# Kernel tuning notes

Measured on AMD Instinct MI355X. Metric: run time of the kernel, lower is better.

Reference implementation:

```python
import jax, jax.numpy as jnp
import numpy as np

EPS = 1e-5
NUM_HEADS = 8
POOL_K = 50
POOL_S = 15
DEPTH = 4


def _conv2d(x, w, b, pad_h, pad_w):
    y = jax.lax.conv_general_dilated(
        x, w, window_strides=(1, 1),
        padding=((pad_h, pad_h), (pad_w, pad_w)),
        dimension_numbers=('NCHW', 'OIHW', 'NCHW'))
    return y + b[None, :, None, None]


def _bn_eval(x, g, b):
    # eval-mode BatchNorm2d with running_mean=0, running_var=1
    s = g / jnp.sqrt(1.0 + EPS)
    return x * s[None, :, None, None] + b[None, :, None, None]


def _layernorm(x, g, b):
    m = x.mean(-1, keepdims=True)
    v = ((x - m) ** 2).mean(-1, keepdims=True)
    return (x - m) / jnp.sqrt(v + EPS) * g + b


def _mha(x, wq, bq, wk, bk, wv, bv, wo, bo):
    B, n, d = x.shape
    def split(h):
        return h.reshape(B, n, NUM_HEADS, -1).transpose(0, 2, 1, 3)  # b h n dk
    q = split(x @ wq.T + bq)
    k = split(x @ wk.T + bk)
    v = split(x @ wv.T + bv)
    dk = q.shape[-1]
    scores = jnp.einsum('bhqd,bhkd->bhqk', q, k) / jnp.sqrt(jnp.float32(dk))
    attn = jax.nn.softmax(scores, axis=-1)
    o = jnp.einsum('bhqk,bhkd->bhqd', attn, v).transpose(0, 2, 1, 3).reshape(B, n, d)
    return o @ wo.T + bo


def _encoder(x, p):
    (g1, b1, g2, b2, wq, bq, wk, bk, wv, bv, wo, bo, f1w, f1b, f2w, f2b) = p
    h = _layernorm(x, g1, b1)
    x = x + _mha(h, wq, bq, wk, bk, wv, bv, wo, bo)
    h = _layernorm(x, g2, b2)
    ff = jax.nn.gelu(h @ f1w.T + f1b, approximate=False) @ f2w.T + f2b
    return x + ff


def _forward(x, tw1, tb1, tw2, tb2, tw3, tb3, tw4, tb4, bn1_g, bn1_b, sw, sb,
             bn2_g, bn2_b, ln1_g, ln1_b, ln2_g, ln2_b, wq, bq, wk, bk, wv, bv,
             wo, bo, f1w, f1b, f2w, f2b, ew, eb, bn3_g, bn3_b, cw, cb):
    B, C, T = x.shape
    xi = x[:, None]  # [B,1,C,T]
    h = jnp.concatenate([
        _conv2d(xi, tw1, tb1, 0, 7),
        _conv2d(xi, tw2, tb2, 0, 12),
        _conv2d(xi, tw3, tb3, 0, 25),
        _conv2d(xi, tw4, tb4, 0, 32)], axis=1)          # [B,D,C,T]
    h = _bn_eval(h, bn1_g, bn1_b)
    h = _conv2d(h, sw, sb, 0, 0)                         # [B,D,1,T]
    h = jax.nn.elu(_bn_eval(h, bn2_g, bn2_b))[:, :, 0]   # [B,D,T]

    npos = (T - POOL_K) // POOL_S + 1
    idx = np.arange(npos)[:, None] * POOL_S + np.arange(POOL_K)  # [n,K]
    win = h[:, :, idx]                                   # [B,D,n,K]
    avg = win.mean(-1)                                   # [B,D,n]
    var = win.var(-1, ddof=1)                            # unbiased, like torch
    vlog = jnp.log(jnp.clip(var, 1e-6, 1e6))
    x1 = avg.transpose(0, 2, 1)                          # [B,n,D]
    x2 = vlog.transpose(0, 2, 1)

    for i in range(DEPTH):
        p = (ln1_g[i], ln1_b[i], ln2_g[i], ln2_b[i], wq[i], bq[i], wk[i], bk[i],
             wv[i], bv[i], wo[i], bo[i], f1w[i], f1b[i], f2w[i], f2b[i])
        x1 = _encoder(x1, p)
        x2 = _encoder(x2, p)

    h = jnp.concatenate([x1[:, :, None, :], x2[:, :, None, :]], axis=2)  # [B,n,2,D]
    h = jax.nn.elu(_bn_eval(_conv2d(h, ew, eb, 0, 0), bn3_g, bn3_b))     # [B,n,1,D]
    return h.reshape(B, -1) @ cw.T + cb


def setup_inputs() -> dict:
    B, C, T, D, n, ff, ncls = 16, 64, 1000, 128, 64, 512, 4
    ks = iter(jax.random.split(jax.random.key(0), 48))
    def nrm(shape, s=0.02):
        return jax.random.normal(next(ks), shape, jnp.float32) * s
    inp = {
        'x': jax.random.normal(next(ks), (B, C, T), jnp.float32),
        'tw1': nrm((D // 4, 1, 1, 15)), 'tb1': jnp.zeros(D // 4),
        'tw2': nrm((D // 4, 1, 1, 25)), 'tb2': jnp.zeros(D // 4),
        'tw3': nrm((D // 4, 1, 1, 51)), 'tb3': jnp.zeros(D // 4),
        'tw4': nrm((D // 4, 1, 1, 65)), 'tb4': jnp.zeros(D // 4),
        'bn1_g': jnp.ones(D), 'bn1_b': jnp.zeros(D),
        'sw': nrm((D, D, C, 1)), 'sb': jnp.zeros(D),
        'bn2_g': jnp.ones(D), 'bn2_b': jnp.zeros(D),
        'ln1_g': jnp.ones((DEPTH, D)), 'ln1_b': jnp.zeros((DEPTH, D)),
        'ln2_g': jnp.ones((DEPTH, D)), 'ln2_b': jnp.zeros((DEPTH, D)),
        'wq': nrm((DEPTH, D, D)), 'bq': jnp.zeros((DEPTH, D)),
        'wk': nrm((DEPTH, D, D)), 'bk': jnp.zeros((DEPTH, D)),
        'wv': nrm((DEPTH, D, D)), 'bv': jnp.zeros((DEPTH, D)),
        'wo': nrm((DEPTH, D, D)), 'bo': jnp.zeros((DEPTH, D)),
        'f1w': nrm((DEPTH, ff, D)), 'f1b': jnp.zeros((DEPTH, ff)),
        'f2w': nrm((DEPTH, D, ff)), 'f2b': jnp.zeros((DEPTH, D)),
        'ew': nrm((n, n, 2, 1)), 'eb': jnp.zeros(n),
        'bn3_g': jnp.ones(n), 'bn3_b': jnp.zeros(n),
        'cw': nrm((ncls, D * n)), 'cb': jnp.zeros(ncls),
    }
    return inp


def reference(x, tw1, tb1, tw2, tb2, tw3, tb3, tw4, tb4, bn1_g, bn1_b, sw, sb,
              bn2_g, bn2_b, ln1_g, ln1_b, ln2_g, ln2_b, wq, bq, wk, bk, wv, bv,
              wo, bo, f1w, f1b, f2w, f2b, ew, eb, bn3_g, bn3_b, cw, cb):
    return _forward(x, tw1, tb1, tw2, tb2, tw3, tb3, tw4, tb4, bn1_g, bn1_b,
                    sw, sb, bn2_g, bn2_b, ln1_g, ln1_b, ln2_g, ln2_b, wq, bq,
                    wk, bk, wv, bv, wo, bo, f1w, f1b, f2w, f2b, ew, eb,
                    bn3_g, bn3_b, cw, cb)
```

## Files before the change

kernel.cpp:

```cpp
#include <hip/hip_runtime.h>
#include <math.h>

typedef unsigned short u16;
typedef __attribute__((ext_vector_type(8))) short frag8;
typedef __attribute__((ext_vector_type(4))) float f32x4;

__device__ __forceinline__ float eluf(float v) { return v > 0.f ? v : expm1f(v); }
__device__ __forceinline__ float geluf(float v) {
  return 0.5f * v * (1.f + erff(v * 0.70710678118654752f));
}
__device__ __forceinline__ u16 f2bf(float f) {
  union { float f; unsigned int i; } v; v.f = f;
  return (u16)((v.i + 0x7fffu + ((v.i >> 16) & 1u)) >> 16);
}

#define BN_S 0.99999500003749969f

__global__ void k_tws1(const float* tw1, const float* tw2, const float* tw3, const float* tw4,
                       const float* tb1, const float* tb2, const float* tb3, const float* tb4,
                       const float* bn1g, const float* bn1b,
                       float* tws1, float* c1) {
  int idx = blockIdx.x * 256 + threadIdx.x;
  if (idx < 8320) {
    int i = idx / 65, u = idx - i * 65;
    int g = i >> 5, il = i & 31;
    const float* tws[4] = {tw1, tw2, tw3, tw4};
    const int P[4] = {7, 12, 25, 32};
    int c = u - 32;
    float s1 = bn1g[i] * BN_S;
    float val = 0.f;
    int p = P[g];
    if (c >= -p && c <= p) val = s1 * tws[g][il * (2 * p + 1) + (c + p)];
    tws1[idx] = val;
  } else if (idx < 8448) {
    int i = idx - 8320;
    int g = i >> 5, il = i & 31;
    const float* tbs[4] = {tb1, tb2, tb3, tb4};
    float s1 = bn1g[i] * BN_S;
    c1[i] = s1 * tbs[g][il] + bn1b[i];
  }
}

__global__ __launch_bounds__(256) void k_weff(const float* __restrict__ sw, const float* __restrict__ sb,
                                              const float* __restrict__ tws1, const float* __restrict__ c1,
                                              u16* __restrict__ Wb, float* __restrict__ biasEff) {
  const int lane = threadIdx.x & 63, wave = threadIdx.x >> 6;
  const int u = blockIdx.x;
  const int o = blockIdx.y * 4 + wave;
  const float* swp = sw + o * 8192 + lane;
  if (u < 65) {
    const float* tp = tws1 + u;
    float a0 = 0.f, a1 = 0.f, a2 = 0.f, a3 = 0.f;
    #pragma unroll 8
    for (int i = 0; i < 128; i += 4) {
      a0 = fmaf(swp[(i + 0) * 64], tp[(i + 0) * 65], a0);
      a1 = fmaf(swp[(i + 1) * 64], tp[(i + 1) * 65], a1);
      a2 = fmaf(swp[(i + 2) * 64], tp[(i + 2) * 65], a2);
      a3 = fmaf(swp[(i + 3) * 64], tp[(i + 3) * 65], a3);
    }
    Wb[(u * 128 + o) * 64 + lane] = f2bf((a0 + a1) + (a2 + a3));
  } else {
    float pa = 0.f;
    #pragma unroll 8
    for (int i = 0; i < 128; i++)
      pa = fmaf(swp[i * 64], c1[i], pa);
    #pragma unroll
    for (int off = 32; off; off >>= 1) pa += __shfl_xor(pa, off);
    if (lane == 0) biasEff[o] = pa + sb[o];
  }
}

__global__ __launch_bounds__(256) void k_conv(const float* __restrict__ x,
                                              const u16* __restrict__ Wb,
                                              const float* __restrict__ biasEff,
                                              const float* __restrict__ bn2g, const float* __restrict__ bn2b,
                                              float* __restrict__ z) {
  __shared__ u16 xs[128 * 88];
  const int tid = threadIdx.x;
  const int t0 = blockIdx.x * 64;
  const int o0 = blockIdx.y * 64;
  const int b  = blockIdx.z;

  #pragma unroll
  for (int i = 0; i < 8; i++) {
    int pos = tid + i * 256;
    int kh = pos >> 5;
    int tt = (pos & 31) * 4;
    int gt = t0 - 32 + tt;
    const float* xp = x + (b * 64 + kh) * 1000;
    float v[4];
    if (gt >= 0 && gt + 3 < 1000) {
      float4 f = *(const float4*)(xp + gt);
      v[0] = f.x; v[1] = f.y; v[2] = f.z; v[3] = f.w;
    } else {
      #pragma unroll
      for (int e = 0; e < 4; e++) { int g2 = gt + e; v[e] = (g2 >= 0 && g2 < 1000) ? xp[g2] : 0.f; }
    }
    #pragma unroll
    for (int e = 0; e < 4; e++) xs[(tt + e) * 88 + kh] = f2bf(v[e]);
  }
  __syncthreads();

  const int lane = tid & 63, wave = tid >> 6;
  const int wt = (wave & 1) * 32;
  const int wo = (wave >> 1) * 32;
  const int m = lane & 15, q = lane >> 4;

  f32x4 acc[2][2];
  #pragma unroll
  for (int i = 0; i < 2; i++)
    #pragma unroll
    for (int j = 0; j < 2; j++) acc[i][j] = (f32x4){0.f, 0.f, 0.f, 0.f};

  #pragma unroll 2
  for (int u = 0; u < 65; u++) {
    frag8 A[2][2], B[2][2];
    #pragma unroll
    for (int tp = 0; tp < 2; tp++)
      #pragma unroll
      for (int kc = 0; kc < 2; kc++)
        A[tp][kc] = *(const frag8*)&xs[(wt + tp * 16 + m + u) * 88 + kc * 32 + q * 8];
    #pragma unroll
    for (int op = 0; op < 2; op++)
      #pragma unroll
      for (int kc = 0; kc < 2; kc++)
        B[op][kc] = *(const frag8*)(Wb + ((u * 128) + o0 + wo + op * 16 + m) * 64 + kc * 32 + q * 8);
    #pragma unroll
    for (int tp = 0; tp < 2; tp++)
      #pragma unroll
      for (int op = 0; op < 2; op++) {
        acc[tp][op] = __builtin_amdgcn_mfma_f32_16x16x32_bf16(A[tp][0], B[op][0], acc[tp][op], 0, 0, 0);
        acc[tp][op] = __builtin_amdgcn_mfma_f32_16x16x32_bf16(A[tp][1], B[op][1], acc[tp][op], 0, 0, 0);
      }
  }

  #pragma unroll
  for (int op = 0; op < 2; op++) {
    int o = o0 + wo + op * 16 + m;
    float s2 = bn2g[o] * BN_S;
    float be = biasEff[o], b2 = bn2b[o];
    #pragma unroll
    for (int tp = 0; tp < 2; tp++) {
      #pragma unroll
      for (int r = 0; r < 4; r++) {
        int t = t0 + wt + tp * 16 + q * 4 + r;
        if (t < 1000)
          z[(b * 128 + o) * 1000 + t] = eluf((acc[tp][op][r] + be) * s2 + b2);
      }
    }
  }
}

__global__ __launch_bounds__(128) void k_pool(const float* __restrict__ z, float* __restrict__ X) {
  int p = blockIdx.x, b = blockIdx.y, o = threadIdx.x;
  const float* zp = z + (b * 128 + o) * 1000 + p * 15;
  float s = 0.f, ss = 0.f;
  #pragma unroll
  for (int k = 0; k < 50; k++) { float v = zp[k]; s += v; ss = fmaf(v, v, ss); }
  float m = s * 0.02f;
  float var = (ss - s * m) * (1.f / 49.f);
  var = fminf(fmaxf(var, 1e-6f), 1e6f);
  X[(b * 64 + p) * 128 + o] = m;
  X[((16 + b) * 64 + p) * 128 + o] = logf(var);
}

__global__ __launch_bounds__(256) void k_cvt6(const float* __restrict__ wq, const float* __restrict__ wk,
                                              const float* __restrict__ wv, const float* __restrict__ wo,
                                              const float* __restrict__ f1w, const float* __restrict__ f2w,
                                              u16* __restrict__ out) {
  int i = blockIdx.x * 256 + threadIdx.x;
  if (i >= 196608) return;
  int fi = i * 4;
  const float* src; int off;
  if      (fi < 65536)  { src = wq;  off = fi; }
  else if (fi < 131072) { src = wk;  off = fi - 65536; }
  else if (fi < 196608) { src = wv;  off = fi - 131072; }
  else if (fi < 262144) { src = wo;  off = fi - 196608; }
  else if (fi < 524288) { src = f1w; off = fi - 262144; }
  else                  { src = f2w; off = fi - 524288; }
  float4 v = *(const float4*)(src + off);
  ushort4 p;
  p.x = f2bf(v.x); p.y = f2bf(v.y); p.z = f2bf(v.z); p.w = f2bf(v.w);
  *(ushort4*)(out + fi) = p;
}

__device__ __forceinline__ void ln128(const float* __restrict__ Xs, u16* __restrict__ Hs,
                                      const float* __restrict__ g, const float* __restrict__ b,
                                      int lane, int wave) {
  float g0 = g[lane], g1 = g[64 + lane], b0 = b[lane], b1 = b[64 + lane];
  #pragma unroll 1
  for (int rr = 0; rr < 8; rr++) {
    int r = wave * 8 + rr;
    float v0 = Xs[r * 132 + lane], v1 = Xs[r * 132 + 64 + lane];
    float s_ = v0 + v1;
    #pragma unroll
    for (int off = 32; off; off >>= 1) s_ += __shfl_xor(s_, off);
    float mn = s_ * (1.f / 128.f);
    float d0 = v0 - mn, d1 = v1 - mn;
    float qq = d0 * d0 + d1 * d1;
    #pragma unroll
    for (int off = 32; off; off >>= 1) qq += __shfl_xor(qq, off);
    float rs = rsqrtf(qq * (1.f / 128.f) + 1e-5f);
    Hs[r * 136 + lane]      = f2bf(d0 * rs * g0 + b0);
    Hs[r * 136 + 64 + lane] = f2bf(d1 * rs * g1 + b1);
  }
}

__device__ __forceinline__ void gemm_tile(const u16* __restrict__ Asrc, int astride,
                                          const u16* __restrict__ Bsrc, int bstride,
                                          int m, int q, f32x4 acc[4]) {
  #pragma unroll
  for (int kc = 0; kc < 4; kc++) {
    frag8 Bf = *(const frag8*)(Bsrc + m * bstride + kc * 32 + q * 8);
    #pragma unroll
    for (int mt = 0; mt < 4; mt++) {
      frag8 Af = *(const frag8*)(Asrc + (mt * 16 + m) * astride + kc * 32 + q * 8);
      acc[mt] = __builtin_amdgcn_mfma_f32_16x16x32_bf16(Af, Bf, acc[mt], 0, 0, 0);
    }
  }
}

__global__ __launch_bounds__(512, 1) void k_enc(float* __restrict__ X,
                                                const u16* __restrict__ Wenc,
                                                const float* __restrict__ ln1g, const float* __restrict__ ln1b,
                                                const float* __restrict__ ln2g, const float* __restrict__ ln2b,
                                                const float* __restrict__ bq, const float* __restrict__ bk,
                                                const float* __restrict__ bv, const float* __restrict__ bo,
                                                const float* __restrict__ f1b, const float* __restrict__ f2b) {
  __shared__ float Xs[64 * 132];
  __shared__ u16   Hs[64 * 136];
  __shared__ float QKV[3 * 64 * 132];
  float* Qs = QKV;
  float* Ks = QKV + 64 * 132;
  float* Vs = QKV + 2 * 64 * 132;
  u16* AOs = (u16*)QKV;
  u16* F1s = (u16*)QKV;

  const int tid = threadIdx.x;
  const int lane = tid & 63, wave = tid >> 6;
  const int m = lane & 15, q = lane >> 4;
  float* Xg = X + blockIdx.x * 64 * 128;

  const u16* WQ  = Wenc;
  const u16* WK  = Wenc + 65536;
  const u16* WV  = Wenc + 131072;
  const u16* WO  = Wenc + 196608;
  const u16* F1W = Wenc + 262144;
  const u16* F2W = Wenc + 524288;

  for (int i = tid; i < 8192; i += 512) Xs[(i >> 7) * 132 + (i & 127)] = Xg[i];
  __syncthreads();

  #pragma unroll 1
  for (int l = 0; l < 4; l++) {
    const u16* wqb  = WQ  + l * 16384;
    const u16* wkb  = WK  + l * 16384;
    const u16* wvb  = WV  + l * 16384;
    const u16* wob  = WO  + l * 16384;
    const u16* f1wb = F1W + l * 65536;
    const u16* f2wb = F2W + l * 65536;
    const int n0 = wave * 16;

    ln128(Xs, Hs, ln1g + l * 128, ln1b + l * 128, lane, wave);
    __syncthreads();

    {
      f32x4 aq[4], ak[4], av[4];
      #pragma unroll
      for (int mt = 0; mt < 4; mt++) { aq[mt] = (f32x4){0,0,0,0}; ak[mt] = (f32x4){0,0,0,0}; av[mt] = (f32x4){0,0,0,0}; }
      gemm_tile(Hs, 136, wqb + n0 * 128, 128, m, q, aq);
      gemm_tile(Hs, 136, wkb + n0 * 128, 128, m, q, ak);
      gemm_tile(Hs, 136, wvb + n0 * 128, 128, m, q, av);
      float bqv = bq[l * 128 + n0 + m];
      float bkv = bk[l * 128 + n0 + m];
      float bvv = bv[l * 128 + n0 + m];
      #pragma unroll
      for (int mt = 0; mt < 4; mt++)
        #pragma unroll
        for (int r = 0; r < 4; r++) {
          int row = mt * 16 + q * 4 + r;
          Qs[row * 132 + n0 + m] = aq[mt][r] + bqv;
          Ks[row * 132 + n0 + m] = ak[mt][r] + bkv;
          Vs[row * 132 + n0 + m] = av[mt][r] + bvv;
        }
    }
    __syncthreads();

    {
      const int h = wave, qr = lane;
      float qv[16];
      {
        const float4* qp = (const float4*)(Qs + qr * 132 + h * 16);
        #pragma unroll
        for (int j = 0; j < 4; j++) {
          float4 t = qp[j];
          qv[j * 4 + 0] = t.x; qv[j * 4 + 1] = t.y; qv[j * 4 + 2] = t.z; qv[j * 4 + 3] = t.w;
        }
      }
      __syncthreads();
      const float* kbase = Ks + h * 16;
      const float* vbase = Vs + h * 16;
      float mrun = -1e30f, lrun = 0.f;
      float o[16];
      #pragma unroll
      for (int j = 0; j < 16; j++) o[j] = 0.f;
      #pragma unroll 1
      for (int k = 0; k < 64; k++) {
        const float4* kp = (const float4*)(kbase + k * 132);
        float4 k0 = kp[0], k1 = kp[1], k2 = kp[2], k3 = kp[3];
        float s0 = qv[0] * k0.x + qv[1] * k0.y + qv[2] * k0.z + qv[3] * k0.w;
        float s1 = qv[4] * k1.x + qv[5] * k1.y + qv[6] * k1.z + qv[7] * k1.w;
        float s2 = qv[8] * k2.x + qv[9] * k2.y + qv[10] * k2.z + qv[11] * k2.w;
        float s3 = qv[12] * k3.x + qv[13] * k3.y + qv[14] * k3.z + qv[15] * k3.w;
        float sc = ((s0 + s1) + (s2 + s3)) * 0.25f;
        float mn = fmaxf(mrun, sc);
        float corr = __expf(mrun - mn);
        float p = __expf(sc - mn);
        lrun = fmaf(lrun, corr, p);
        const float4* vp = (const float4*)(vbase + k * 132);
        float4 v0 = vp[0], v1 = vp[1], v2 = vp[2], v3 = vp[3];
        o[0]  = fmaf(o[0],  corr, p * v0.x); o[1]  = fmaf(o[1],  corr, p * v0.y);
        o[2]  = fmaf(o[2],  corr, p * v0.z); o[3]  = fmaf(o[3],  corr, p * v0.w);
        o[4]  = fmaf(o[4],  corr, p * v1.x); o[5]  = fmaf(o[5],  corr, p * v1.y);
        o[6]  = fmaf(o[6],  corr, p * v1.z); o[7]  = fmaf(o[7],  corr, p * v1.w);
        o[8]  = fmaf(o[8],  corr, p * v2.x); o[9]  = fmaf(o[9],  corr, p * v2.y);
        o[10] = fmaf(o[10], corr, p * v2.z); o[11] = fmaf(o[11], corr, p * v2.w);
        o[12] = fmaf(o[12], corr, p * v3.x); o[13] = fmaf(o[13], corr, p * v3.y);
        o[14] = fmaf(o[14], corr, p * v3.z); o[15] = fmaf(o[15], corr, p * v3.w);
        mrun = mn;
      }
      float inv = 1.f / lrun;
      u16* aop = AOs + qr * 136 + h * 16;
      #pragma unroll
      for (int j = 0; j < 16; j++) aop[j] = f2bf(o[j] * inv);
    }
    __syncthreads();

    {
      f32x4 acc[4];
      #pragma unroll
      for (int mt = 0; mt < 4; mt++) acc[mt] = (f32x4){0,0,0,0};
      gemm_tile(AOs, 136, wob + n0 * 128, 128, m, q, acc);
      float bvv = bo[l * 128 + n0 + m];
      #pragma unroll
      for (int mt = 0; mt < 4; mt++)
        #pragma unroll
        for (int r = 0; r < 4; r++)
          Xs[(mt * 16 + q * 4 + r) * 132 + n0 + m] += acc[mt][r] + bvv;
    }
    __syncthreads();

    ln128(Xs, Hs, ln2g + l * 128, ln2b + l * 128, lane, wave);
    __syncthreads();

    {
      f32x4 acc2[4];
      #pragma unroll
      for (int mt = 0; mt < 4; mt++) acc2[mt] = (f32x4){0,0,0,0};
      #pragma unroll 1
      for (int c = 0; c < 4; c++) {
        f32x4 a1[4];
        #pragma unroll
        for (int mt = 0; mt < 4; mt++) a1[mt] = (f32x4){0,0,0,0};
        gemm_tile(Hs, 136, f1wb + (c * 128 + n0) * 128, 128, m, q, a1);
        float b1v = f1b[l * 512 + c * 128 + n0 + m];
        #pragma unroll
        for (int mt = 0; mt < 4; mt++)
          #pragma unroll
          for (int r = 0; r < 4; r++)
            F1s[(mt * 16 + q * 4 + r) * 136 + n0 + m] = f2bf(geluf(a1[mt][r] + b1v));
        __syncthreads();
        gemm_tile(F1s, 136, f2wb + n0 * 512 + c * 128, 512, m, q, acc2);
        __syncthreads();
      }
      float b2v = f2b[l * 128 + n0 + m];
      #pragma unroll
      for (int mt = 0; mt < 4; mt++)
        #pragma unroll
        for (int r = 0; r < 4; r++)
          Xs[(mt * 16 + q * 4 + r) * 132 + n0 + m] += acc2[mt][r] + b2v;
    }
    __syncthreads();
  }

  for (int i = tid; i < 8192; i += 512) Xg[i] = Xs[(i >> 7) * 132 + (i & 127)];
}

__global__ __launch_bounds__(256) void k_head1(const float* __restrict__ X, const float* __restrict__ ew,
                                               const float* __restrict__ eb, const float* __restrict__ g3,
                                               const float* __restrict__ b3, float* __restrict__ G) {
  __shared__ float Xs[2][8192];
  int b = blockIdx.x, ot = blockIdx.y;
  int tid = threadIdx.x;
  {
    const float4* x1 = (const float4*)(X + b * 8192);
    const float4* x2 = (const float4*)(X + (16 + b) * 8192);
    float4* s1 = (float4*)&Xs[0][0];
    float4* s2 = (float4*)&Xs[1][0];
    for (int i = tid; i < 2048; i += 256) { s1[i] = x1[i]; s2[i] = x2[i]; }
  }
  __syncthreads();
  int w = tid & 127, og = tid >> 7;
  int oc0 = ot * 16 + og * 8;
  float a[8] = {};
  for (int ic = 0; ic < 64; ic++) {
    float x1v = Xs[0][ic * 128 + w], x2v = Xs[1][ic * 128 + w];
    #pragma unroll
    for (int j = 0; j < 8; j++) {
      a[j] = fmaf(ew[((oc0 + j) * 64 + ic) * 2 + 0], x1v, a[j]);
      a[j] = fmaf(ew[((oc0 + j) * 64 + ic) * 2 + 1], x2v, a[j]);
    }
  }
  #pragma unroll
  for (int j = 0; j < 8; j++) {
    int oc = oc0 + j;
    float v = (a[j] + eb[oc]) * (g3[oc] * BN_S) + b3[oc];
    G[(b * 64 + oc) * 128 + w] = eluf(v);
  }
}

__global__ __launch_bounds__(256) void k_head2(const float* __restrict__ G, const float* __restrict__ cw,
                                               const float* __restrict__ cb, float* __restrict__ out) {
  __shared__ float red[256];
  int b = blockIdx.x, c = blockIdx.y, tid = threadIdx.x;
  const float4* g4 = (const float4*)(G + b * 8192);
  const float4* c4 = (const float4*)(cw + c * 8192);
  float p = 0.f;
  for (int i = tid; i < 2048; i += 256) {
    float4 g = g4[i], w = c4[i];
    p += g.x * w.x + g.y * w.y + g.z * w.z + g.w * w.w;
  }
  red[tid] = p;
  __syncthreads();
  for (int s = 128; s > 0; s >>= 1) {
    if (tid < s) red[tid] += red[tid + s];
    __syncthreads();
  }
  if (tid == 0) out[b * 4 + c] = red[0] + cb[c];
}

extern "C" void kernel_launch(void* const* d_in, const int* in_sizes, int n_in,
                              void* d_out, int out_size, void* d_ws, size_t ws_size,
                              hipStream_t stream) {
  const float* x    = (const float*)d_in[0];
  const float* tw1  = (const float*)d_in[1];  const float* tb1 = (const float*)d_in[2];
  const float* tw2  = (const float*)d_in[3];  const float* tb2 = (const float*)d_in[4];
  const float* tw3  = (const float*)d_in[5];  const float* tb3 = (const float*)d_in[6];
  const float* tw4  = (const float*)d_in[7];  const float* tb4 = (const float*)d_in[8];
  const float* bn1g = (const float*)d_in[9];  const float* bn1b = (const float*)d_in[10];
  const float* sw   = (const float*)d_in[11]; const float* sb   = (const float*)d_in[12];
  const float* bn2g = (const float*)d_in[13]; const float* bn2b = (const float*)d_in[14];
  const float* ln1g = (const float*)d_in[15]; const float* ln1b = (const float*)d_in[16];
  const float* ln2g = (const float*)d_in[17]; const float* ln2b = (const float*)d_in[18];
  const float* wq   = (const float*)d_in[19]; const float* bq   = (const float*)d_in[20];
  const float* wk   = (const float*)d_in[21]; const float* bk   = (const float*)d_in[22];
  const float* wv   = (const float*)d_in[23]; const float* bv   = (const float*)d_in[24];
  const float* wo   = (const float*)d_in[25]; const float* bo   = (const float*)d_in[26];
  const float* f1w  = (const float*)d_in[27]; const float* f1b  = (const float*)d_in[28];
  const float* f2w  = (const float*)d_in[29]; const float* f2b  = (const float*)d_in[30];
  const float* ew   = (const float*)d_in[31]; const float* eb   = (const float*)d_in[32];
  const float* g3   = (const float*)d_in[33]; const float* b3   = (const float*)d_in[34];
  const float* cw   = (const float*)d_in[35]; const float* cb   = (const float*)d_in[36];

  float* ws      = (float*)d_ws;
  float* tws1    = ws;
  float* c1      = ws + 8320;
  float* biasEff = ws + 8448;
  u16*   Wb      = (u16*)(ws + 8576);
  float* z       = ws + 541056;
  float* X       = ws + 2589056;
  u16*   Wenc    = (u16*)(ws + 3113344);
  float* G       = z;

  k_cvt6<<<768, 256, 0, stream>>>(wq, wk, wv, wo, f1w, f2w, Wenc);
  k_tws1<<<33, 256, 0, stream>>>(tw1, tw2, tw3, tw4, tb1, tb2, tb3, tb4, bn1g, bn1b, tws1, c1);
  k_weff<<<dim3(66, 32), 256, 0, stream>>>(sw, sb, tws1, c1, Wb, biasEff);
  k_conv<<<dim3(16, 2, 16), 256, 0, stream>>>(x, Wb, biasEff, bn2g, bn2b, z);
  k_pool<<<dim3(64, 16), 128, 0, stream>>>(z, X);

  k_enc<<<32, 512, 0, stream>>>(X, Wenc, ln1g, ln1b, ln2g, ln2b, bq, bk, bv, bo, f1b, f2b);

  k_head1<<<dim3(16, 4), 256, 0, stream>>>(X, ew, eb, g3, b3, G);
  k_head2<<<dim3(16, 4), 256, 0, stream>>>(G, cw, cb, (float*)d_out);
}
```

Measured before the change: 420.8 us.

## Double encoder block threads and halve conv output tile per block

Measured after the change: 454.1 us. 1.08x slower.

```diff
diff --git a/kernel.cpp b/kernel.cpp
--- a/kernel.cpp
+++ b/kernel.cpp
@@ -78,7 +78,7 @@
   __shared__ u16 xs[128 * 88];
   const int tid = threadIdx.x;
   const int t0 = blockIdx.x * 64;
-  const int o0 = blockIdx.y * 64;
+  const int o0 = blockIdx.y * 32;
   const int b  = blockIdx.z;
 
   #pragma unroll
@@ -103,40 +103,33 @@
 
   const int lane = tid & 63, wave = tid >> 6;
   const int wt = (wave & 1) * 32;
-  const int wo = (wave >> 1) * 32;
+  const int wo = (wave >> 1) * 16;
   const int m = lane & 15, q = lane >> 4;
 
-  f32x4 acc[2][2];
+  f32x4 acc[2];
   #pragma unroll
-  for (int i = 0; i < 2; i++)
-    #pragma unroll
-    for (int j = 0; j < 2; j++) acc[i][j] = (f32x4){0.f, 0.f, 0.f, 0.f};
+  for (int i = 0; i < 2; i++) acc[i] = (f32x4){0.f, 0.f, 0.f, 0.f};
 
   #pragma unroll 2
   for (int u = 0; u < 65; u++) {
-    frag8 A[2][2], B[2][2];
+    frag8 A[2][2], B[2];
     #pragma unroll
     for (int tp = 0; tp < 2; tp++)
       #pragma unroll
       for (int kc = 0; kc < 2; kc++)
         A[tp][kc] = *(const frag8*)&xs[(wt + tp * 16 + m + u) * 88 + kc * 32 + q * 8];
     #pragma unroll
-    for (int op = 0; op < 2; op++)
-      #pragma unroll
-      for (int kc = 0; kc < 2; kc++)
-        B[op][kc] = *(const frag8*)(Wb + ((u * 128) + o0 + wo + op * 16 + m) * 64 + kc * 32 + q * 8);
-    #pragma unroll
-    for (int tp = 0; tp < 2; tp++)
-      #pragma unroll
-      for (int op = 0; op < 2; op++) {
-        acc[tp][op] = __builtin_amdgcn_mfma_f32_16x16x32_bf16(A[tp][0], B[op][0], acc[tp][op], 0, 0, 0);
-        acc[tp][op] = __builtin_amdgcn_mfma_f32_16x16x32_bf16(A[tp][1], B[op][1], acc[tp][op], 0, 0, 0);
-      }
-  }
-
-  #pragma unroll
-  for (int op = 0; op < 2; op++) {
-    int o = o0 + wo + op * 16 + m;
+    for (int kc = 0; kc < 2; kc++)
+      B[kc] = *(const frag8*)(Wb + ((u * 128) + o0 + wo + m) * 64 + kc * 32 + q * 8);
+    #pragma unroll
+    for (int tp = 0; tp < 2; tp++) {
+      acc[tp] = __builtin_amdgcn_mfma_f32_16x16x32_bf16(A[tp][0], B[0], acc[tp], 0, 0, 0);
+      acc[tp] = __builtin_amdgcn_mfma_f32_16x16x32_bf16(A[tp][1], B[1], acc[tp], 0, 0, 0);
+    }
+  }
+
+  {
+    int o = o0 + wo + m;
     float s2 = bn2g[o] * BN_S;
     float be = biasEff[o], b2 = bn2b[o];
     #pragma unroll
@@ -145,7 +138,7 @@
       for (int r = 0; r < 4; r++) {
         int t = t0 + wt + tp * 16 + q * 4 + r;
         if (t < 1000)
-          z[(b * 128 + o) * 1000 + t] = eluf((acc[tp][op][r] + be) * s2 + b2);
+          z[(b * 128 + o) * 1000 + t] = eluf((acc[tp][r] + be) * s2 + b2);
       }
     }
   }
@@ -189,8 +182,8 @@
                                       int lane, int wave) {
   float g0 = g[lane], g1 = g[64 + lane], b0 = b[lane], b1 = b[64 + lane];
   #pragma unroll 1
-  for (int rr = 0; rr < 8; rr++) {
-    int r = wave * 8 + rr;
+  for (int rr = 0; rr < 4; rr++) {
+    int r = wave * 4 + rr;
     float v0 = Xs[r * 132 + lane], v1 = Xs[r * 132 + 64 + lane];
     float s_ = v0 + v1;
     #pragma unroll
@@ -206,35 +199,22 @@
   }
 }
 
-__device__ __forceinline__ void gemm_tile(const u16* __restrict__ Asrc, int astride,
-                                          const u16* __restrict__ Bsrc, int bstride,
-                                          int m, int q, f32x4 acc[4]) {
-  #pragma unroll
-  for (int kc = 0; kc < 4; kc++) {
-    frag8 Bf = *(const frag8*)(Bsrc + m * bstride + kc * 32 + q * 8);
-    #pragma unroll
-    for (int mt = 0; mt < 4; mt++) {
-      frag8 Af = *(const frag8*)(Asrc + (mt * 16 + m) * astride + kc * 32 + q * 8);
-      acc[mt] = __builtin_amdgcn_mfma_f32_16x16x32_bf16(Af, Bf, acc[mt], 0, 0, 0);
-    }
-  }
-}
-
-__global__ __launch_bounds__(512, 1) void k_enc(float* __restrict__ X,
-                                                const u16* __restrict__ Wenc,
-                                                const float* __restrict__ ln1g, const float* __restrict__ ln1b,
-                                                const float* __restrict__ ln2g, const float* __restrict__ ln2b,
-                                                const float* __restrict__ bq, const float* __restrict__ bk,
-                                                const float* __restrict__ bv, const float* __restrict__ bo,
-                                                const float* __restrict__ f1b, const float* __restrict__ f2b) {
+__global__ __launch_bounds__(1024, 1) void k_enc(float* __restrict__ X,
+                                                 const u16* __restrict__ Wenc,
+                                                 const float* __restrict__ ln1g, const float* __restrict__ ln1b,
+                                                 const float* __restrict__ ln2g, const float* __restrict__ ln2b,
+                                                 const float* __restrict__ bq, const float* __restrict__ bk,
+                                                 const float* __restrict__ bv, const float* __restrict__ bo,
+                                                 const float* __restrict__ f1b, const float* __restrict__ f2b) {
   __shared__ float Xs[64 * 132];
   __shared__ u16   Hs[64 * 136];
   __shared__ float QKV[3 * 64 * 132];
   float* Qs = QKV;
   float* Ks = QKV + 64 * 132;
   float* Vs = QKV + 2 * 64 * 132;
-  u16* AOs = (u16*)QKV;
-  u16* F1s = (u16*)QKV;
+  u16* AOs = Hs;
+  u16* F1a = (u16*)QKV;
+  u16* F1b_ = (u16*)QKV + 64 * 136;
 
   const int tid = threadIdx.x;
   const int lane = tid & 63, wave = tid >> 6;
@@ -248,7 +228,7 @@
   const u16* F1W = Wenc + 262144;
   const u16* F2W = Wenc + 524288;
 
-  for (int i = tid; i < 8192; i += 512) Xs[(i >> 7) * 132 + (i & 127)] = Xg[i];
+  for (int i = tid; i < 8192; i += 1024) Xs[(i >> 7) * 132 + (i & 127)] = Xg[i];
   __syncthreads();
 
   #pragma unroll 1
@@ -259,34 +239,39 @@
     const u16* wob  = WO  + l * 16384;
     const u16* f1wb = F1W + l * 65536;
     const u16* f2wb = F2W + l * 65536;
-    const int n0 = wave * 16;
 
     ln128(Xs, Hs, ln1g + l * 128, ln1b + l * 128, lane, wave);
     __syncthreads();
 
-    {
-      f32x4 aq[4], ak[4], av[4];
-      #pragma unroll
-      for (int mt = 0; mt < 4; mt++) { aq[mt] = (f32x4){0,0,0,0}; ak[mt] = (f32x4){0,0,0,0}; av[mt] = (f32x4){0,0,0,0}; }
-      gemm_tile(Hs, 136, wqb + n0 * 128, 128, m, q, aq);
-      gemm_tile(Hs, 136, wkb + n0 * 128, 128, m, q, ak);
-      gemm_tile(Hs, 136, wvb + n0 * 128, 128, m, q, av);
-      float bqv = bq[l * 128 + n0 + m];
-      float bkv = bk[l * 128 + n0 + m];
-      float bvv = bv[l * 128 + n0 + m];
-      #pragma unroll
-      for (int mt = 0; mt < 4; mt++)
-        #pragma unroll
-        for (int r = 0; r < 4; r++) {
-          int row = mt * 16 + q * 4 + r;
-          Qs[row * 132 + n0 + m] = aq[mt][r] + bqv;
-          Ks[row * 132 + n0 + m] = ak[mt][r] + bkv;
-          Vs[row * 132 + n0 + m] = av[mt][r] + bvv;
+    #pragma unroll
+    for (int s = 0; s < 3; s++) {
+      int uidx = wave * 3 + s;
+      int ns = uidx >> 1, mh = uidx & 1;
+      int which = ns >> 3, nsl = ns & 7;
+      const u16* Bp = (which == 0 ? wqb : which == 1 ? wkb : wvb) + (nsl * 16) * 128;
+      float* Dst = (which == 0 ? Qs : which == 1 ? Ks : Vs);
+      const float* bptr = (which == 0 ? bq : which == 1 ? bk : bv) + l * 128;
+      f32x4 a2[2];
+      a2[0] = (f32x4){0,0,0,0}; a2[1] = (f32x4){0,0,0,0};
+      #pragma unroll
+      for (int kc = 0; kc < 4; kc++) {
+        frag8 Bf = *(const frag8*)(Bp + m * 128 + kc * 32 + q * 8);
+        #pragma unroll
+        for (int t = 0; t < 2; t++) {
+          frag8 Af = *(const frag8*)&Hs[(mh * 32 + t * 16 + m) * 136 + kc * 32 + q * 8];
+          a2[t] = __builtin_amdgcn_mfma_f32_16x16x32_bf16(Af, Bf, a2[t], 0, 0, 0);
         }
-    }
-    __syncthreads();
-
-    {
+      }
+      float bvv = bptr[nsl * 16 + m];
+      #pragma unroll
+      for (int t = 0; t < 2; t++)
+        #pragma unroll
+        for (int r = 0; r < 4; r++)
+          Dst[(mh * 32 + t * 16 + q * 4 + r) * 132 + nsl * 16 + m] = a2[t][r] + bvv;
+    }
+    __syncthreads();
+
+    if (wave < 8) {
       const int h = wave, qr = lane;
       float qv[16];
       {
@@ -297,7 +282,6 @@
           qv[j * 4 + 0] = t.x; qv[j * 4 + 1] = t.y; qv[j * 4 + 2] = t.z; qv[j * 4 + 3] = t.w;
         }
       }
-      __syncthreads();
       const float* kbase = Ks + h * 16;
       const float* vbase = Vs + h * 16;
       float mrun = -1e30f, lrun = 0.f;
@@ -337,16 +321,25 @@
     __syncthreads();
 
     {
-      f32x4 acc[4];
-      #pragma unroll
-      for (int mt = 0; mt < 4; mt++) acc[mt] = (f32x4){0,0,0,0};
-      gemm_tile(AOs, 136, wob + n0 * 128, 128, m, q, acc);
-      float bvv = bo[l * 128 + n0 + m];
-      #pragma unroll
-      for (int mt = 0; mt < 4; mt++)
+      int ns = wave >> 1, mh = wave & 1;
+      const u16* Bp = wob + (ns * 16) * 128;
+      f32x4 a2[2];
+      a2[0] = (f32x4){0,0,0,0}; a2[1] = (f32x4){0,0,0,0};
+      #pragma unroll
+      for (int kc = 0; kc < 4; kc++) {
+        frag8 Bf = *(const frag8*)(Bp + m * 128 + kc * 32 + q * 8);
+        #pragma unroll
+        for (int t = 0; t < 2; t++) {
+          frag8 Af = *(const frag8*)&AOs[(mh * 32 + t * 16 + m) * 136 + kc * 32 + q * 8];
+          a2[t] = __builtin_amdgcn_mfma_f32_16x16x32_bf16(Af, Bf, a2[t], 0, 0, 0);
+        }
+      }
+      float bvv = bo[l * 128 + ns * 16 + m];
+      #pragma unroll
+      for (int t = 0; t < 2; t++)
         #pragma unroll
         for (int r = 0; r < 4; r++)
-          Xs[(mt * 16 + q * 4 + r) * 132 + n0 + m] += acc[mt][r] + bvv;
+          Xs[(mh * 32 + t * 16 + q * 4 + r) * 132 + ns * 16 + m] += a2[t][r] + bvv;
     }
     __syncthreads();
 
@@ -354,36 +347,57 @@
     __syncthreads();
 
     {
-      f32x4 acc2[4];
-      #pragma unroll
-      for (int mt = 0; mt < 4; mt++) acc2[mt] = (f32x4){0,0,0,0};
+      int ns = wave >> 1, mh = wave & 1;
+      f32x4 acc2[2];
+      acc2[0] = (f32x4){0,0,0,0}; acc2[1] = (f32x4){0,0,0,0};
       #pragma unroll 1
       for (int c = 0; c < 4; c++) {
-        f32x4 a1[4];
-        #pragma unroll
-        for (int mt = 0; mt < 4; mt++) a1[mt] = (f32x4){0,0,0,0};
-        gemm_tile(Hs, 136, f1wb + (c * 128 + n0) * 128, 128, m, q, a1);
-        float b1v = f1b[l * 512 + c * 128 + n0 + m];
-        #pragma unroll
-        for (int mt = 0; mt < 4; mt++)
+        u16* F1c = (c & 1) ? F1b_ : F1a;
+        {
+          const u16* Bp = f1wb + (c * 128 + ns * 16) * 128;
+          f32x4 a1[2];
+          a1[0] = (f32x4){0,0,0,0}; a1[1] = (f32x4){0,0,0,0};
           #pragma unroll
-          for (int r = 0; r < 4; r++)
-            F1s[(mt * 16 + q * 4 + r) * 136 + n0 + m] = f2bf(geluf(a1[mt][r] + b1v));
+          for (int kc = 0; kc < 4; kc++) {
+            frag8 Bf = *(const frag8*)(Bp + m * 128 + kc * 32 + q * 8);
+            #pragma unroll
+            for (int t = 0; t < 2; t++) {
+              frag8 Af = *(const frag8*)&Hs[(mh * 32 + t * 16 + m) * 136 + kc * 32 + q * 8];
+              a1[t] = __builtin_amdgcn_mfma_f32_16x16x32_bf16(Af, Bf, a1[t], 0, 0, 0);
+            }
+          }
+          float b1v = f1b[l * 512 + c * 128 + ns * 16 + m];
+          #pragma unroll
+          for (int t = 0; t < 2; t++)
+            #pragma unroll
+            for (int r = 0; r < 4; r++)
+              F1c[(mh * 32 + t * 16 + q * 4 + r) * 136 + ns * 16 + m] = f2bf(geluf(a1[t][r] + b1v));
+        }
         __syncthreads();
-        gemm_tile(F1s, 136, f2wb + n0 * 512 + c * 128, 512, m, q, acc2);
-        __syncthreads();
-      }
-      float b2v = f2b[l * 128 + n0 + m];
-      #pragma unroll
-      for (int mt = 0; mt < 4; mt++)
+        {
+          const u16* Bp = f2wb + (ns * 16) * 512 + c * 128;
+          #pragma unroll
+          for (int kc = 0; kc < 4; kc++) {
+            frag8 Bf = *(const frag8*)(Bp + m * 512 + kc * 32 + q * 8);
+            #pragma unroll
+            for (int t = 0; t < 2; t++) {
+              frag8 Af = *(const frag8*)&F1c[(mh * 32 + t * 16 + m) * 136 + kc * 32 + q * 8];
+              acc2[t] = __builtin_amdgcn_mfma_f32_16x16x32_bf16(Af, Bf, acc2[t], 0, 0, 0);
+            }
+          }
+        }
+      }
+      float b2v = f2b[l * 128 + ns * 16 + m];
+      #pragma unroll
+      for (int t = 0; t < 2; t++)
         #pragma unroll
         for (int r = 0; r < 4; r++)
-          Xs[(mt * 16 + q * 4 + r) * 132 + n0 + m] += acc2[mt][r] + b2v;
-    }
-    __syncthreads();
-  }
-
-  for (int i = tid; i < 8192; i += 512) Xg[i] = Xs[(i >> 7) * 132 + (i & 127)];
+          Xs[(mh * 32 + t * 16 + q * 4 + r) * 132 + ns * 16 + m] += acc2[t][r] + b2v;
+    }
+    __syncthreads();
+  }
+
+  for (int i = tid; i < 8192; i += 1024) Xg[i] = Xs[(i >> 7) * 132 + (i & 127)];
 }
 
 __global__ __launch_bounds__(256) void k_head1(const float* __restrict__ X, const float* __restrict__ ew,
@@ -475,10 +489,10 @@
   k_cvt6<<<768, 256, 0, stream>>>(wq, wk, wv, wo, f1w, f2w, Wenc);
   k_tws1<<<33, 256, 0, stream>>>(tw1, tw2, tw3, tw4, tb1, tb2, tb3, tb4, bn1g, bn1b, tws1, c1);
   k_weff<<<dim3(66, 32), 256, 0, stream>>>(sw, sb, tws1, c1, Wb, biasEff);
-  k_conv<<<dim3(16, 2, 16), 256, 0, stream>>>(x, Wb, biasEff, bn2g, bn2b, z);
+  k_conv<<<dim3(16, 4, 16), 256, 0, stream>>>(x, Wb, biasEff, bn2g, bn2b, z);
   k_pool<<<dim3(64, 16), 128, 0, stream>>>(z, X);
 
-  k_enc<<<32, 512, 0, stream>>>(X, Wenc, ln1g, ln1b, ln2g, ln2b, bq, bk, bv, bo, f1b, f2b);
+  k_enc<<<32, 1024, 0, stream>>>(X, Wenc, ln1g, ln1b, ln2g, ln2b, bq, bk, bv, bo, f1b, f2b);
 
   k_head1<<<dim3(16, 4), 256, 0, stream>>>(X, ew, eb, g3, b3, G);
   k_head2<<<dim3(16, 4), 256, 0, stream>>>(G, cw, cb, (float*)d_out);
```
